# Optimization experiments

Measured on AMD Instinct MI355X. Metric: run time of the kernel, lower is better.

The kernel has to match this reference:

```python
import jax, jax.numpy as jnp
import numpy as np

BINS = 256

def setup_inputs() -> dict:
    key = jax.random.key(0)
    x = jax.random.normal(key, (64, 3, 512, 512), dtype=jnp.float32)
    return {"x": x}

def reference(x):
    bins = BINS

    def equalize_one(img):
        # img: (C, H, W) -- flattened wholesale, matching the torch per-index loop
        flat = img.reshape(-1)
        mn = flat.min()
        mx = flat.max()
        norm = (flat - mn) * (bins - 1) / (mx - mn + 1e-8)
        norm = jnp.clip(norm, 0, bins - 1)
        idx = norm.astype(jnp.int32)  # bucket index per pixel
        hist = jnp.zeros((bins,), jnp.float32).at[idx].add(1.0)  # bincount
        cdf = jnp.cumsum(hist)
        cdf_norm = (cdf - cdf.min()) / (cdf.max() - cdf.min() + 1e-8)
        return cdf_norm[idx].reshape(img.shape)  # gather equalized values

    return jax.vmap(equalize_one)(x)
```

## Files before the change

kernel.cpp:

```cpp
#include <hip/hip_runtime.h>

#define NUM_BINS 256
#define NPI (3*512*512)
#define TPB 256
#define MM_BLOCKS 16
#define NSUB 16
#define SUBSTRIDE 257
#define G_VEC 4

__device__ __forceinline__ unsigned fmap(float f) {
  unsigned u = __float_as_uint(f);
  return (u & 0x80000000u) ? ~u : (u | 0x80000000u);
}
__device__ __forceinline__ float funmap(unsigned m) {
  unsigned u = (m & 0x80000000u) ? (m ^ 0x80000000u) : ~m;
  return __uint_as_float(u);
}

__device__ __forceinline__ int bin_of(float v, float mn, float denom) {
  float norm = (v - mn) * 255.0f / denom;
  norm = fminf(fmaxf(norm, 0.0f), 255.0f);
  return (int)norm;
}

__global__ void init_ws(unsigned* __restrict__ minmax, int* __restrict__ hist) {
  int b = blockIdx.x;
  hist[b * NUM_BINS + threadIdx.x] = 0;
  if (threadIdx.x == 0) { minmax[2*b] = 0xFFFFFFFFu; minmax[2*b+1] = 0u; }
}

__global__ void minmax_k(const float4* __restrict__ x, unsigned* __restrict__ minmax) {
  const int chunk4 = NPI / 4 / MM_BLOCKS;
  int img = blockIdx.x / MM_BLOCKS;
  int blk = blockIdx.x % MM_BLOCKS;
  const float4* p = x + (size_t)img * (NPI/4) + (size_t)blk * chunk4;
  float mn = 3.4e38f, mx = -3.4e38f;
  for (int i = threadIdx.x; i < chunk4; i += TPB) {
    float4 v = p[i];
    mn = fminf(mn, fminf(fminf(v.x, v.y), fminf(v.z, v.w)));
    mx = fmaxf(mx, fmaxf(fmaxf(v.x, v.y), fmaxf(v.z, v.w)));
  }
  for (int off = 32; off > 0; off >>= 1) {
    mn = fminf(mn, __shfl_down(mn, off));
    mx = fmaxf(mx, __shfl_down(mx, off));
  }
  __shared__ float smn[4], smx[4];
  int wave = threadIdx.x >> 6, lane = threadIdx.x & 63;
  if (lane == 0) { smn[wave] = mn; smx[wave] = mx; }
  __syncthreads();
  if (threadIdx.x == 0) {
    mn = fminf(fminf(smn[0], smn[1]), fminf(smn[2], smn[3]));
    mx = fmaxf(fmaxf(smx[0], smx[1]), fmaxf(smx[2], smx[3]));
    atomicMin(&minmax[2*img],   fmap(mn));
    atomicMax(&minmax[2*img+1], fmap(mx));
  }
}

__global__ void hist_k(const float4* __restrict__ x,
                       const unsigned* __restrict__ minmax,
                       int* __restrict__ hist) {
  __shared__ int sh[NSUB * SUBSTRIDE];
  for (int i = threadIdx.x; i < NSUB * SUBSTRIDE; i += TPB) sh[i] = 0;
  const int chunk4 = NPI / 4 / MM_BLOCKS;
  int img = blockIdx.x / MM_BLOCKS;
  int blk = blockIdx.x % MM_BLOCKS;
  float mn = funmap(minmax[2*img]);
  float mx = funmap(minmax[2*img+1]);
  float denom = mx - mn + 1e-8f;
  __syncthreads();
  const float4* p = x + (size_t)img * (NPI/4) + (size_t)blk * chunk4;
  int* mysub = sh + (threadIdx.x % NSUB) * SUBSTRIDE;
  for (int i = threadIdx.x; i < chunk4; i += TPB * 4) {
    float4 v0 = p[i];
    float4 v1 = p[i + TPB];
    float4 v2 = p[i + 2*TPB];
    float4 v3 = p[i + 3*TPB];
    atomicAdd(&mysub[bin_of(v0.x, mn, denom)], 1);
    atomicAdd(&mysub[bin_of(v0.y, mn, denom)], 1);
    atomicAdd(&mysub[bin_of(v0.z, mn, denom)], 1);
    atomicAdd(&mysub[bin_of(v0.w, mn, denom)], 1);
    atomicAdd(&mysub[bin_of(v1.x, mn, denom)], 1);
    atomicAdd(&mysub[bin_of(v1.y, mn, denom)], 1);
    atomicAdd(&mysub[bin_of(v1.z, mn, denom)], 1);
    atomicAdd(&mysub[bin_of(v1.w, mn, denom)], 1);
    atomicAdd(&mysub[bin_of(v2.x, mn, denom)], 1);
    atomicAdd(&mysub[bin_of(v2.y, mn, denom)], 1);
    atomicAdd(&mysub[bin_of(v2.z, mn, denom)], 1);
    atomicAdd(&mysub[bin_of(v2.w, mn, denom)], 1);
    atomicAdd(&mysub[bin_of(v3.x, mn, denom)], 1);
    atomicAdd(&mysub[bin_of(v3.y, mn, denom)], 1);
    atomicAdd(&mysub[bin_of(v3.z, mn, denom)], 1);
    atomicAdd(&mysub[bin_of(v3.w, mn, denom)], 1);
  }
  __syncthreads();
  int bin = threadIdx.x;
  int s = 0;
  #pragma unroll
  for (int c = 0; c < NSUB; ++c) s += sh[c * SUBSTRIDE + bin];
  atomicAdd(&hist[img * NUM_BINS + bin], s);
}

__global__ void scan_k(const int* __restrict__ hist, float* __restrict__ cdfn) {
  __shared__ int s[NUM_BINS];
  int img = blockIdx.x, t = threadIdx.x;
  s[t] = hist[img * NUM_BINS + t];
  __syncthreads();
  for (int off = 1; off < NUM_BINS; off <<= 1) {
    int add = (t >= off) ? s[t - off] : 0;
    __syncthreads();
    s[t] += add;
    __syncthreads();
  }
  int cdf = s[t], c0 = s[0], cN = s[NUM_BINS - 1];
  cdfn[img * NUM_BINS + t] = (float)(cdf - c0) / ((float)(cN - c0) + 1e-8f);
}

__global__ void gather_k(const float4* __restrict__ x,
                         const unsigned* __restrict__ minmax,
                         const float* __restrict__ cdfn,
                         float4* __restrict__ out) {
  __shared__ float c[NUM_BINS];
  const int f4pi = NPI / 4;
  const int CHUNK = TPB * G_VEC;
  const int bpi = f4pi / CHUNK;
  int img = blockIdx.x / bpi;
  int blk = blockIdx.x % bpi;
  c[threadIdx.x] = cdfn[img * NUM_BINS + threadIdx.x];
  float mn = funmap(minmax[2*img]);
  float denom = funmap(minmax[2*img+1]) - mn + 1e-8f;
  __syncthreads();
  size_t base = (size_t)img * f4pi + (size_t)blk * CHUNK + threadIdx.x;
  #pragma unroll
  for (int j = 0; j < G_VEC; ++j) {
    float4 v = x[base + (size_t)j * TPB];
    float4 o;
    o.x = c[bin_of(v.x, mn, denom)];
    o.y = c[bin_of(v.y, mn, denom)];
    o.z = c[bin_of(v.z, mn, denom)];
    o.w = c[bin_of(v.w, mn, denom)];
    out[base + (size_t)j * TPB] = o;
  }
}

extern "C" void kernel_launch(void* const* d_in, const int* in_sizes, int n_in,
                              void* d_out, int out_size, void* d_ws, size_t ws_size,
                              hipStream_t stream) {
  const float* x = (const float*)d_in[0];
  float* out = (float*)d_out;
  int B = in_sizes[0] / NPI;

  unsigned* minmax = (unsigned*)d_ws;
  int* hist  = (int*)((char*)d_ws + (size_t)2 * B * sizeof(unsigned));
  float* cdfn = (float*)((char*)d_ws + (size_t)2 * B * sizeof(unsigned)
                                      + (size_t)B * NUM_BINS * sizeof(int));

  init_ws<<<B, NUM_BINS, 0, stream>>>(minmax, hist);
  minmax_k<<<B * MM_BLOCKS, TPB, 0, stream>>>((const float4*)x, minmax);
  hist_k<<<B * MM_BLOCKS, TPB, 0, stream>>>((const float4*)x, minmax, hist);
  scan_k<<<B, NUM_BINS, 0, stream>>>(hist, cdfn);
  gather_k<<<B * (NPI/4/(TPB*G_VEC)), TPB, 0, stream>>>((const float4*)x, minmax, cdfn, (float4*)out);
}
```

Measured before the change: 400.6 us.

## Fuse init and scan into neighbours, use per-block minmax partials

Drops the init and scan kernels. Workspace zeroing moves into the minmax kernel, and the scan runs in the last-arriving histogram block through a done counter and threadfence. Global float atomics for min/max are replaced by per-block partials that each consumer reduces, and the minmax kernel uses more blocks with two accumulators. Histogram privatisation changes from 16 thread-interleaved sub-histograms to 4 per-wave copies, which may add shared-atomic contention. The intent is to remove two launches and the atomic serialisation.

Measured after the change: 503.0 us. +25.6%, slower.

```diff
diff --git a/kernel.cpp b/kernel.cpp
--- a/kernel.cpp
+++ b/kernel.cpp
@@ -3,19 +3,10 @@
 #define NUM_BINS 256
 #define NPI (3*512*512)
 #define TPB 256
-#define MM_BLOCKS 16
-#define NSUB 16
-#define SUBSTRIDE 257
-#define G_VEC 4
-
-__device__ __forceinline__ unsigned fmap(float f) {
-  unsigned u = __float_as_uint(f);
-  return (u & 0x80000000u) ? ~u : (u | 0x80000000u);
-}
-__device__ __forceinline__ float funmap(unsigned m) {
-  unsigned u = (m & 0x80000000u) ? (m ^ 0x80000000u) : ~m;
-  return __uint_as_float(u);
-}
+#define NIMG 64
+#define MMB 32
+#define HB 16
+#define GVEC 4
 
 __device__ __forceinline__ int bin_of(float v, float mn, float denom) {
   float norm = (v - mn) * 255.0f / denom;
@@ -23,23 +14,23 @@
   return (int)norm;
 }
 
-__global__ void init_ws(unsigned* __restrict__ minmax, int* __restrict__ hist) {
-  int b = blockIdx.x;
-  hist[b * NUM_BINS + threadIdx.x] = 0;
-  if (threadIdx.x == 0) { minmax[2*b] = 0xFFFFFFFFu; minmax[2*b+1] = 0u; }
-}
+__global__ void minmax_k(const float4* __restrict__ x, float2* __restrict__ partials,
+                         int* __restrict__ hist, int* __restrict__ done) {
+  const int chunk4 = NPI / 4 / MMB;
+  int img = blockIdx.x / MMB;
+  int blk = blockIdx.x % MMB;
+  const float4* p = x + (size_t)img * (NPI/4) + (size_t)blk * chunk4;
 
-__global__ void minmax_k(const float4* __restrict__ x, unsigned* __restrict__ minmax) {
-  const int chunk4 = NPI / 4 / MM_BLOCKS;
-  int img = blockIdx.x / MM_BLOCKS;
-  int blk = blockIdx.x % MM_BLOCKS;
-  const float4* p = x + (size_t)img * (NPI/4) + (size_t)blk * chunk4;
-  float mn = 3.4e38f, mx = -3.4e38f;
-  for (int i = threadIdx.x; i < chunk4; i += TPB) {
-    float4 v = p[i];
-    mn = fminf(mn, fminf(fminf(v.x, v.y), fminf(v.z, v.w)));
-    mx = fmaxf(mx, fmaxf(fmaxf(v.x, v.y), fmaxf(v.z, v.w)));
+  float mn0 = 3.4e38f, mx0 = -3.4e38f, mn1 = 3.4e38f, mx1 = -3.4e38f;
+  for (int i = threadIdx.x; i < chunk4; i += TPB * 2) {
+    float4 a = p[i];
+    float4 b = p[i + TPB];
+    mn0 = fminf(mn0, fminf(fminf(a.x, a.y), fminf(a.z, a.w)));
+    mx0 = fmaxf(mx0, fmaxf(fmaxf(a.x, a.y), fmaxf(a.z, a.w)));
+    mn1 = fminf(mn1, fminf(fminf(b.x, b.y), fminf(b.z, b.w)));
+    mx1 = fmaxf(mx1, fmaxf(fmaxf(b.x, b.y), fmaxf(b.z, b.w)));
   }
+  float mn = fminf(mn0, mn1), mx = fmaxf(mx0, mx1);
   for (int off = 32; off > 0; off >>= 1) {
     mn = fminf(mn, __shfl_down(mn, off));
     mx = fmaxf(mx, __shfl_down(mx, off));
@@ -51,87 +42,105 @@
   if (threadIdx.x == 0) {
     mn = fminf(fminf(smn[0], smn[1]), fminf(smn[2], smn[3]));
     mx = fmaxf(fmaxf(smx[0], smx[1]), fmaxf(smx[2], smx[3]));
-    atomicMin(&minmax[2*img],   fmap(mn));
-    atomicMax(&minmax[2*img+1], fmap(mx));
+    partials[blockIdx.x] = make_float2(mn, mx);
+  }
+  if (blockIdx.x < NIMG) {
+    hist[blockIdx.x * NUM_BINS + threadIdx.x] = 0;
+    if (threadIdx.x == 0) done[blockIdx.x] = 0;
   }
 }
 
-__global__ void hist_k(const float4* __restrict__ x,
-                       const unsigned* __restrict__ minmax,
-                       int* __restrict__ hist) {
-  __shared__ int sh[NSUB * SUBSTRIDE];
-  for (int i = threadIdx.x; i < NSUB * SUBSTRIDE; i += TPB) sh[i] = 0;
-  const int chunk4 = NPI / 4 / MM_BLOCKS;
-  int img = blockIdx.x / MM_BLOCKS;
-  int blk = blockIdx.x % MM_BLOCKS;
-  float mn = funmap(minmax[2*img]);
-  float mx = funmap(minmax[2*img+1]);
+__global__ void hist_k(const float4* __restrict__ x, const float2* __restrict__ partials,
+                       int* __restrict__ hist, int* __restrict__ done,
+                       float* __restrict__ cdfn) {
+  __shared__ int wh[4 * NUM_BINS];
+  __shared__ int sdone;
+  const int chunk4 = NPI / 4 / HB;
+  int img = blockIdx.x / HB;
+  int blk = blockIdx.x % HB;
+
+  float mn = 3.4e38f, mx = -3.4e38f;
+  for (int j = 0; j < MMB; ++j) {
+    float2 pm = partials[img * MMB + j];
+    mn = fminf(mn, pm.x);
+    mx = fmaxf(mx, pm.y);
+  }
   float denom = mx - mn + 1e-8f;
+
+  for (int i = threadIdx.x; i < 4 * NUM_BINS; i += TPB) wh[i] = 0;
   __syncthreads();
+
+  int* myh = wh + (threadIdx.x >> 6) * NUM_BINS;
   const float4* p = x + (size_t)img * (NPI/4) + (size_t)blk * chunk4;
-  int* mysub = sh + (threadIdx.x % NSUB) * SUBSTRIDE;
   for (int i = threadIdx.x; i < chunk4; i += TPB * 4) {
     float4 v0 = p[i];
     float4 v1 = p[i + TPB];
     float4 v2 = p[i + 2*TPB];
     float4 v3 = p[i + 3*TPB];
-    atomicAdd(&mysub[bin_of(v0.x, mn, denom)], 1);
-    atomicAdd(&mysub[bin_of(v0.y, mn, denom)], 1);
-    atomicAdd(&mysub[bin_of(v0.z, mn, denom)], 1);
-    atomicAdd(&mysub[bin_of(v0.w, mn, denom)], 1);
-    atomicAdd(&mysub[bin_of(v1.x, mn, denom)], 1);
-    atomicAdd(&mysub[bin_of(v1.y, mn, denom)], 1);
-    atomicAdd(&mysub[bin_of(v1.z, mn, denom)], 1);
-    atomicAdd(&mysub[bin_of(v1.w, mn, denom)], 1);
-    atomicAdd(&mysub[bin_of(v2.x, mn, denom)], 1);
-    atomicAdd(&mysub[bin_of(v2.y, mn, denom)], 1);
-    atomicAdd(&mysub[bin_of(v2.z, mn, denom)], 1);
-    atomicAdd(&mysub[bin_of(v2.w, mn, denom)], 1);
-    atomicAdd(&mysub[bin_of(v3.x, mn, denom)], 1);
-    atomicAdd(&mysub[bin_of(v3.y, mn, denom)], 1);
-    atomicAdd(&mysub[bin_of(v3.z, mn, denom)], 1);
-    atomicAdd(&mysub[bin_of(v3.w, mn, denom)], 1);
+    atomicAdd(&myh[bin_of(v0.x, mn, denom)], 1);
+    atomicAdd(&myh[bin_of(v0.y, mn, denom)], 1);
+    atomicAdd(&myh[bin_of(v0.z, mn, denom)], 1);
+    atomicAdd(&myh[bin_of(v0.w, mn, denom)], 1);
+    atomicAdd(&myh[bin_of(v1.x, mn, denom)], 1);
+    atomicAdd(&myh[bin_of(v1.y, mn, denom)], 1);
+    atomicAdd(&myh[bin_of(v1.z, mn, denom)], 1);
+    atomicAdd(&myh[bin_of(v1.w, mn, denom)], 1);
+    atomicAdd(&myh[bin_of(v2.x, mn, denom)], 1);
+    atomicAdd(&myh[bin_of(v2.y, mn, denom)], 1);
+    atomicAdd(&myh[bin_of(v2.z, mn, denom)], 1);
+    atomicAdd(&myh[bin_of(v2.w, mn, denom)], 1);
+    atomicAdd(&myh[bin_of(v3.x, mn, denom)], 1);
+    atomicAdd(&myh[bin_of(v3.y, mn, denom)], 1);
+    atomicAdd(&myh[bin_of(v3.z, mn, denom)], 1);
+    atomicAdd(&myh[bin_of(v3.w, mn, denom)], 1);
   }
   __syncthreads();
-  int bin = threadIdx.x;
-  int s = 0;
-  #pragma unroll
-  for (int c = 0; c < NSUB; ++c) s += sh[c * SUBSTRIDE + bin];
-  atomicAdd(&hist[img * NUM_BINS + bin], s);
+
+  int t = threadIdx.x;
+  int s = wh[t] + wh[NUM_BINS + t] + wh[2*NUM_BINS + t] + wh[3*NUM_BINS + t];
+  atomicAdd(&hist[img * NUM_BINS + t], s);
+  __syncthreads();
+  __threadfence();
+  if (t == 0) sdone = atomicAdd(&done[img], 1);
+  __syncthreads();
+
+  if (sdone == HB - 1) {
+    int* sh = wh;
+    sh[t] = atomicAdd(&hist[img * NUM_BINS + t], 0);
+    __syncthreads();
+    for (int off = 1; off < NUM_BINS; off <<= 1) {
+      int add = (t >= off) ? sh[t - off] : 0;
+      __syncthreads();
+      sh[t] += add;
+      __syncthreads();
+    }
+    int cdf = sh[t], c0 = sh[0], cN = sh[NUM_BINS - 1];
+    cdfn[img * NUM_BINS + t] = (float)(cdf - c0) / ((float)(cN - c0) + 1e-8f);
+  }
 }
 
-__global__ void scan_k(const int* __restrict__ hist, float* __restrict__ cdfn) {
-  __shared__ int s[NUM_BINS];
-  int img = blockIdx.x, t = threadIdx.x;
-  s[t] = hist[img * NUM_BINS + t];
-  __syncthreads();
-  for (int off = 1; off < NUM_BINS; off <<= 1) {
-    int add = (t >= off) ? s[t - off] : 0;
-    __syncthreads();
-    s[t] += add;
-    __syncthreads();
-  }
-  int cdf = s[t], c0 = s[0], cN = s[NUM_BINS - 1];
-  cdfn[img * NUM_BINS + t] = (float)(cdf - c0) / ((float)(cN - c0) + 1e-8f);
-}
-
-__global__ void gather_k(const float4* __restrict__ x,
-                         const unsigned* __restrict__ minmax,
-                         const float* __restrict__ cdfn,
-                         float4* __restrict__ out) {
+__global__ void gather_k(const float4* __restrict__ x, const float2* __restrict__ partials,
+                         const float* __restrict__ cdfn, float4* __restrict__ out) {
   __shared__ float c[NUM_BINS];
   const int f4pi = NPI / 4;
-  const int CHUNK = TPB * G_VEC;
+  const int CHUNK = TPB * GVEC;
   const int bpi = f4pi / CHUNK;
   int img = blockIdx.x / bpi;
   int blk = blockIdx.x % bpi;
   c[threadIdx.x] = cdfn[img * NUM_BINS + threadIdx.x];
-  float mn = funmap(minmax[2*img]);
-  float denom = funmap(minmax[2*img+1]) - mn + 1e-8f;
+
+  float mn = 3.4e38f, mx = -3.4e38f;
+  for (int j = 0; j < MMB; ++j) {
+    float2 pm = partials[img * MMB + j];
+    mn = fminf(mn, pm.x);
+    mx = fmaxf(mx, pm.y);
+  }
+  float denom = mx - mn + 1e-8f;
   __syncthreads();
+
   size_t base = (size_t)img * f4pi + (size_t)blk * CHUNK + threadIdx.x;
   #pragma unroll
-  for (int j = 0; j < G_VEC; ++j) {
+  for (int j = 0; j < GVEC; ++j) {
     float4 v = x[base + (size_t)j * TPB];
     float4 o;
     o.x = c[bin_of(v.x, mn, denom)];
@@ -145,18 +154,16 @@
 extern "C" void kernel_launch(void* const* d_in, const int* in_sizes, int n_in,
                               void* d_out, int out_size, void* d_ws, size_t ws_size,
                               hipStream_t stream) {
-  const float* x = (const float*)d_in[0];
-  float* out = (float*)d_out;
-  int B = in_sizes[0] / NPI;
+  const float4* x = (const float4*)d_in[0];
+  float4* out = (float4*)d_out;
 
-  unsigned* minmax = (unsigned*)d_ws;
-  int* hist  = (int*)((char*)d_ws + (size_t)2 * B * sizeof(unsigned));
-  float* cdfn = (float*)((char*)d_ws + (size_t)2 * B * sizeof(unsigned)
-                                      + (size_t)B * NUM_BINS * sizeof(int));
+  char* w = (char*)d_ws;
+  float2* partials = (float2*)w;                    w += (size_t)NIMG * MMB * sizeof(float2);
+  int*    hist     = (int*)w;                       w += (size_t)NIMG * NUM_BINS * sizeof(int);
+  int*    done     = (int*)w;                       w += (size_t)NIMG * sizeof(int);
+  float*  cdfn     = (float*)w;
 
-  init_ws<<<B, NUM_BINS, 0, stream>>>(minmax, hist);
-  minmax_k<<<B * MM_BLOCKS, TPB, 0, stream>>>((const float4*)x, minmax);
-  hist_k<<<B * MM_BLOCKS, TPB, 0, stream>>>((const float4*)x, minmax, hist);
-  scan_k<<<B, NUM_BINS, 0, stream>>>(hist, cdfn);
-  gather_k<<<B * (NPI/4/(TPB*G_VEC)), TPB, 0, stream>>>((const float4*)x, minmax, cdfn, (float4*)out);
+  minmax_k<<<NIMG * MMB, TPB, 0, stream>>>(x, partials, hist, done);
+  hist_k  <<<NIMG * HB,  TPB, 0, stream>>>(x, partials, hist, done, cdfn);
+  gather_k<<<NIMG * (NPI/4/(TPB*GVEC)), TPB, 0, stream>>>(x, partials, cdfn, out);
 }
```
